# Optimization experiments

Measured on AMD Instinct MI355X. Metric: run time of the kernel, lower is better.

## Reference

```python
import jax, jax.numpy as jnp
import numpy as np

N_NODES = 50000


def gcn_conv(x, W, b, src, dst, ew, n):
    """PyG-style GCNConv: D^-1/2 (A+I) D^-1/2 X W + b with self-loops of weight 1."""
    h = x @ W                                   # [N, out]
    loop = jnp.arange(n, dtype=src.dtype)
    s = jnp.concatenate([src, loop])            # [E+N]
    d = jnp.concatenate([dst, loop])
    w = jnp.concatenate([ew, jnp.ones((n,), dtype=x.dtype)])
    deg = jax.ops.segment_sum(w, d, num_segments=n)
    dinv = jnp.where(deg > 0, jax.lax.rsqrt(deg), 0.0)
    norm = dinv[s] * w * dinv[d]                # [E+N]
    out = jax.ops.segment_sum(h[s] * norm[:, None], d, num_segments=n)
    return out + b


def setup_inputs() -> dict:
    key = jax.random.key(0)
    ks = jax.random.split(key, 12)
    in_feats, hidden = 128, 128
    half = hidden // 2
    E = 800000
    x = jax.random.normal(ks[0], (N_NODES, in_feats), dtype=jnp.float32)
    edge_index = jax.random.randint(ks[1], (2, E), 0, N_NODES, dtype=jnp.int64)
    edge_weight = jax.random.uniform(ks[2], (E,), dtype=jnp.float32)
    def lin(k, fan_in, shape):
        bound = 1.0 / np.sqrt(fan_in)
        return jax.random.uniform(k, shape, minval=-bound, maxval=bound, dtype=jnp.float32)
    return {
        "x": x,
        "edge_index": edge_index,
        "edge_weight": edge_weight,
        "W1": lin(ks[3], in_feats, (in_feats, hidden)),
        "b1": jnp.zeros((hidden,), jnp.float32),
        "W2": lin(ks[4], hidden, (hidden, hidden)),
        "b2": jnp.zeros((hidden,), jnp.float32),
        "Ws": lin(ks[5], in_feats, (in_feats, hidden)),
        "bs": lin(ks[6], in_feats, (hidden,)),
        "Wl": lin(ks[7], in_feats, (in_feats, half)),
        "bl": jnp.zeros((half,), jnp.float32),
        "Wl2": lin(ks[8], half, (half, 1)),
        "bl2": lin(ks[9], half, (1,)),
    }


def reference(x, edge_index, edge_weight, W1, b1, W2, b2, Ws, bs, Wl, bl, Wl2, bl2):
    n = x.shape[0]
    src, dst = edge_index[0], edge_index[1]
    # conv1 + ReLU over neighbors
    h_neighbors = jax.nn.relu(gcn_conv(x, W1, b1, src, dst, edge_weight, n))
    # leader score: GCNConv -> ReLU -> Linear(.,1) -> sigmoid, per node
    ls_h = jax.nn.relu(gcn_conv(x, Wl, bl, src, dst, edge_weight, n))
    leader_score = jax.nn.sigmoid(ls_h @ Wl2 + bl2)        # [N, 1]
    # gated fusion of self projection vs neighbor aggregation
    h_self_proj = x @ Ws + bs
    h_new = (1.0 - leader_score) * h_neighbors + leader_score * h_self_proj
    h_final = jax.nn.relu(gcn_conv(h_new, W2, b2, src, dst, edge_weight, n))
    return (h_final, leader_score)
```

## Files before the change

### kernel.cpp

```cpp
#include <hip/hip_runtime.h>
#include <math.h>

#define THREADS 256
#define ELLS 96
#define NEDGEBLK 1024
#define GEMM_YSTRIDE 104

typedef unsigned int uint32;
typedef unsigned long long ull64;
typedef __attribute__((ext_vector_type(8))) short bf16x8;
typedef __attribute__((ext_vector_type(4))) float f32x4;
typedef __attribute__((ext_vector_type(2))) float f32x2;

__device__ __forceinline__ unsigned short f2bf_rne(float x) {
  uint32 u = __float_as_uint(x);
  u += 0x7fffu + ((u >> 16) & 1u);
  return (unsigned short)(u >> 16);
}

__device__ __forceinline__ f32x2 dw2f2(uint32 d) {
  f32x2 r;
  r.x = __uint_as_float(d << 16);
  r.y = __uint_as_float(d & 0xffff0000u);
  return r;
}


__global__ __launch_bounds__(256) void prep_fused(ull64* __restrict__ packed, int n,
                                                  const float* __restrict__ W1, const float* __restrict__ Wl,
                                                  const float* __restrict__ Ws, const float* __restrict__ W2,
                                                  unsigned short* __restrict__ whi, unsigned short* __restrict__ wlo,
                                                  const float* __restrict__ x, unsigned short* __restrict__ xraw,
                                                  int nInit, int nW) {
  int b = blockIdx.x;
  int t = threadIdx.x;
  if (b < nInit) {
    int i = b * 256 + t;
    if (i < n) packed[i] = 0ull;
  } else if (b < nInit + nW) {
    int idx = (b - nInit) * 256 + t;
    if (idx >= 448 * 128) return;
    int slot = idx >> 7;
    int k = idx & 127;
    const float* W; int ncol, ncols;
    if (slot < 128)      { W = W1; ncol = slot;       ncols = 128; }
    else if (slot < 192) { W = Wl; ncol = slot - 128; ncols = 64;  }
    else if (slot < 320) { W = Ws; ncol = slot - 192; ncols = 128; }
    else                 { W = W2; ncol = slot - 320; ncols = 128; }
    float v = W[(size_t)k * ncols + ncol];
    unsigned short hi = f2bf_rne(v);
    float hif = __uint_as_float((uint32)hi << 16);
    unsigned short lo = f2bf_rne(v - hif);
    whi[idx] = hi;
    wlo[idx] = lo;
  } else {
    int i = (b - nInit - nW) * 256 + t;
    if (i >= n * 16) return;
    const float* px = x + (size_t)i * 8;
    float4 a = *(const float4*)px;
    float4 c = *(const float4*)(px + 4);
    ushort4 r0, r1;
    r0.x = f2bf_rne(a.x); r0.y = f2bf_rne(a.y); r0.z = f2bf_rne(a.z); r0.w = f2bf_rne(a.w);
    r1.x = f2bf_rne(c.x); r1.y = f2bf_rne(c.y); r1.z = f2bf_rne(c.z); r1.w = f2bf_rne(c.w);
    *(ushort4*)(xraw + (size_t)i * 8) = r0;
    *(ushort4*)(xraw + (size_t)i * 8 + 4) = r1;
  }
}


__global__ __launch_bounds__(256) void finalize_kernel(const ull64* __restrict__ packed,
                                                       float* __restrict__ dinv, int* __restrict__ cnt32, int n) {
  int i = blockIdx.x * 256 + threadIdx.x;
  if (i >= n) return;
  const float S = 1.1920928955078125e-7f;
  ull64 p = packed[i];
  dinv[i] = rsqrtf(1.0f + (float)(uint32)(p & 0xffffffffull) * S);
  cnt32[i] = (int)(p >> 32);
}


struct Chunk {
  const unsigned short* A;
  const unsigned short* whi;
  const unsigned short* wlo;
  const float* bias;
  void* out;
  int ostride;
  int obf16;
};
struct GemmArgs { Chunk c[5]; };

__device__ __forceinline__ void gemm_body(const Chunk& d, int M, int nTiles, int tile0, int tstride) {
  const unsigned short* A = d.A;
  int w = threadIdx.x >> 6, lane = threadIdx.x & 63;
  int n16 = lane & 15, quad = lane >> 4;

  bf16x8 Bh[4][4], Bl[4][4];
  {
    const unsigned short* wh = d.whi + (size_t)n16 * 128 + quad * 8;
    const unsigned short* wl = d.wlo + (size_t)n16 * 128 + quad * 8;
#pragma unroll
    for (int ct = 0; ct < 4; ct++)
#pragma unroll
      for (int ks = 0; ks < 4; ks++) {
        Bh[ct][ks] = *(const bf16x8*)(wh + ct * 16 * 128 + ks * 32);
        Bl[ct][ks] = *(const bf16x8*)(wl + ct * 16 * 128 + ks * 32);
      }
  }
  float bv[4];
#pragma unroll
  for (int ct = 0; ct < 4; ct++) bv[ct] = d.bias ? d.bias[ct * 16 + n16] : 0.f;

  int tile = tile0;
  bf16x8 av0[4], av1[4];
  if (tile < nTiles) {
    int bm = tile * 128;
    int r0 = bm + w * 32 + n16, r1 = r0 + 16;
    int r0c = r0 < M ? r0 : M - 1;
    int r1c = r1 < M ? r1 : M - 1;
    const unsigned short* a0 = A + (size_t)r0c * 128 + quad * 8;
    const unsigned short* a1 = A + (size_t)r1c * 128 + quad * 8;
#pragma unroll
    for (int ks = 0; ks < 4; ks++) {
      av0[ks] = *(const bf16x8*)(a0 + ks * 32);
      av1[ks] = *(const bf16x8*)(a1 + ks * 32);
    }
  }

  for (; tile < nTiles; tile += tstride) {
    int nxt = tile + tstride;
    bf16x8 nv0[4], nv1[4];
    if (nxt < nTiles) {
      int bm = nxt * 128;
      int r0 = bm + w * 32 + n16, r1 = r0 + 16;
      int r0c = r0 < M ? r0 : M - 1;
      int r1c = r1 < M ? r1 : M - 1;
      const unsigned short* a0 = A + (size_t)r0c * 128 + quad * 8;
      const unsigned short* a1 = A + (size_t)r1c * 128 + quad * 8;
#pragma unroll
      for (int ks = 0; ks < 4; ks++) {
        nv0[ks] = *(const bf16x8*)(a0 + ks * 32);
        nv1[ks] = *(const bf16x8*)(a1 + ks * 32);
      }
    }

    f32x4 acc[2][4];
#pragma unroll
    for (int rt = 0; rt < 2; rt++)
#pragma unroll
      for (int ct = 0; ct < 4; ct++) acc[rt][ct] = (f32x4){0.f, 0.f, 0.f, 0.f};

#pragma unroll
    for (int ks = 0; ks < 4; ks++)
#pragma unroll
      for (int ct = 0; ct < 4; ct++) {
        acc[0][ct] = __builtin_amdgcn_mfma_f32_16x16x32_bf16(av0[ks], Bh[ct][ks], acc[0][ct], 0, 0, 0);
        acc[0][ct] = __builtin_amdgcn_mfma_f32_16x16x32_bf16(av0[ks], Bl[ct][ks], acc[0][ct], 0, 0, 0);
        acc[1][ct] = __builtin_amdgcn_mfma_f32_16x16x32_bf16(av1[ks], Bh[ct][ks], acc[1][ct], 0, 0, 0);
        acc[1][ct] = __builtin_amdgcn_mfma_f32_16x16x32_bf16(av1[ks], Bl[ct][ks], acc[1][ct], 0, 0, 0);
      }

    int bm = tile * 128;
#pragma unroll
    for (int ct = 0; ct < 4; ct++) {
      int col = ct * 16 + n16;
#pragma unroll
      for (int rt = 0; rt < 2; rt++) {
#pragma unroll
        for (int reg = 0; reg < 4; reg++) {
          int row = bm + w * 32 + rt * 16 + quad * 4 + reg;
          if (row < M) {
            float v = acc[rt][ct][reg] + bv[ct];
            if (d.obf16)
              ((unsigned short*)d.out)[(size_t)row * d.ostride + col] = f2bf_rne(v);
            else
              ((float*)d.out)[(size_t)row * d.ostride + col] = v;
          }
        }
      }
    }

#pragma unroll
    for (int ks = 0; ks < 4; ks++) { av0[ks] = nv0[ks]; av1[ks] = nv1[ks]; }
  }
}

__global__ __launch_bounds__(256, 2) void gemm_v3(GemmArgs args, int M, int nTiles) {
  gemm_body(args.c[blockIdx.x], M, nTiles, blockIdx.y, gridDim.y);
}


__global__ __launch_bounds__(256, 2) void fused_sg(GemmArgs args, int M, int nTiles, int nGemm,
                                                   const int* __restrict__ ei, const float* __restrict__ ew,
                                                   ull64* __restrict__ packed, int2* __restrict__ ell, int E) {
  int b = blockIdx.x;
  int gemmIdx = -1, edgeIdx = -1;
  int twice = nGemm * 2;
  if (b < twice) {
    if (b & 1) gemmIdx = b >> 1; else edgeIdx = b >> 1;
  } else {
    edgeIdx = nGemm + (b - twice);
  }

  if (edgeIdx >= 0) {
    int per = (E + NEDGEBLK - 1) / NEDGEBLK;
    int start = edgeIdx * per;
    int end = start + per;
    if (end > E) end = E;
    for (int e = start + (int)threadIdx.x; e < end; e += 256) {
      int s = ei[e];
      int d = ei[E + e];
      float w = ew[e];
      uint32 fx = (uint32)(w * 8388608.0f + 0.5f);
      ull64 old = atomicAdd(packed + d, (1ull << 32) | (ull64)fx);
      int slot = (int)(old >> 32);
      if (slot < ELLS)
        ell[(size_t)d * ELLS + slot] = make_int2(s, __float_as_int(w));
    }
    return;
  }

  int chunkId = gemmIdx % 5;
  int ytile = gemmIdx / 5;
  gemm_body(args.c[chunkId], M, nTiles, ytile, GEMM_YSTRIDE);
}


__global__ __launch_bounds__(256) void conv1_fused(const unsigned short* __restrict__ h1,
                                                   const unsigned short* __restrict__ hl,
                                                   const int* __restrict__ cnt,
                                                   const int2* __restrict__ csr,
                                                   const float* __restrict__ dinv,
                                                   const float* __restrict__ b1, const float* __restrict__ bl,
                                                   const float* __restrict__ Wl2, const float* __restrict__ bl2,
                                                   const unsigned short* __restrict__ hself,
                                                   unsigned short* __restrict__ hnew_out,
                                                   float* __restrict__ leader_out, int nnodes) {
  int wave = threadIdx.x >> 6;
  int lane = threadIdx.x & 63;
  int node = blockIdx.x * 4 + wave;
  if (node >= nnodes) return;
  int g = lane >> 4, q = lane & 15;
  bool ql = q < 8;
  int hq = q & 7;
  int rs = node * ELLS;
  int n = cnt[node];
  float di = dinv[node];
  f32x2 dv2 = {di, di};

  f32x2 acc1[4] = {};
  f32x2 accl[4] = {};
  if (g == 0) {
    uint4 v = *(const uint4*)(h1 + (size_t)node * 128 + 8 * q);
    acc1[0] = dv2 * dw2f2(v.x); acc1[1] = dv2 * dw2f2(v.y);
    acc1[2] = dv2 * dw2f2(v.z); acc1[3] = dv2 * dw2f2(v.w);
    if (ql) {
      uint4 vl = *(const uint4*)(hl + (size_t)node * 64 + 8 * q);
      accl[0] = dv2 * dw2f2(vl.x); accl[1] = dv2 * dw2f2(vl.y);
      accl[2] = dv2 * dw2f2(vl.z); accl[3] = dv2 * dw2f2(vl.w);
    }
  }

  int e = g;
  for (; e + 4 < n; e += 8) {
    int2 en0 = csr[rs + e];
    int2 en1 = csr[rs + e + 4];
    float wz0 = __int_as_float(en0.y) * dinv[en0.x];
    float wz1 = __int_as_float(en1.y) * dinv[en1.x];
    f32x2 w0 = {wz0, wz0};
    f32x2 w1 = {wz1, wz1};
    uint4 a0 = *(const uint4*)(h1 + (size_t)en0.x * 128 + 8 * q);
    uint4 a1 = *(const uint4*)(h1 + (size_t)en1.x * 128 + 8 * q);
    int srcl = ql ? en0.x : en1.x;
    float wzl = ql ? wz0 : wz1;
    uint4 c0 = *(const uint4*)(hl + (size_t)srcl * 64 + 8 * hq);
    f32x2 wl2 = {wzl, wzl};
    accl[0] += wl2 * dw2f2(c0.x);
    accl[1] += wl2 * dw2f2(c0.y);
    accl[2] += wl2 * dw2f2(c0.z);
    accl[3] += wl2 * dw2f2(c0.w);
    acc1[0] += w0 * dw2f2(a0.x) + w1 * dw2f2(a1.x);
    acc1[1] += w0 * dw2f2(a0.y) + w1 * dw2f2(a1.y);
    acc1[2] += w0 * dw2f2(a0.z) + w1 * dw2f2(a1.z);
    acc1[3] += w0 * dw2f2(a0.w) + w1 * dw2f2(a1.w);
  }
  if (e < n) {
    int2 en = csr[rs + e];
    float wz0 = __int_as_float(en.y) * dinv[en.x];
    f32x2 w0 = {wz0, wz0};
    uint4 a0 = *(const uint4*)(h1 + (size_t)en.x * 128 + 8 * q);
    float wzl = ql ? wz0 : 0.f;
    uint4 c0 = *(const uint4*)(hl + (size_t)en.x * 64 + 8 * hq);
    f32x2 wl2 = {wzl, wzl};
    accl[0] += wl2 * dw2f2(c0.x);
    accl[1] += wl2 * dw2f2(c0.y);
    accl[2] += wl2 * dw2f2(c0.z);
    accl[3] += wl2 * dw2f2(c0.w);
    acc1[0] += w0 * dw2f2(a0.x);
    acc1[1] += w0 * dw2f2(a0.y);
    acc1[2] += w0 * dw2f2(a0.z);
    acc1[3] += w0 * dw2f2(a0.w);
  }

#pragma unroll
  for (int k = 0; k < 4; k++) {
    acc1[k].x += __shfl_xor(acc1[k].x, 16);
    acc1[k].y += __shfl_xor(acc1[k].y, 16);
    acc1[k].x += __shfl_xor(acc1[k].x, 32);
    acc1[k].y += __shfl_xor(acc1[k].y, 32);
    accl[k].x += __shfl_xor(accl[k].x, 16);
    accl[k].y += __shfl_xor(accl[k].y, 16);
    accl[k].x += __shfl_xor(accl[k].x, 32);
    accl[k].y += __shfl_xor(accl[k].y, 32);
    accl[k].x += __shfl_xor(accl[k].x, 8);
    accl[k].y += __shfl_xor(accl[k].y, 8);
  }

  float part = 0.f;
  if (ql) {
    float b[8], w2[8];
    *(float4*)&b[0] = *(const float4*)(bl + 8 * q);
    *(float4*)&b[4] = *(const float4*)(bl + 8 * q + 4);
    *(float4*)&w2[0] = *(const float4*)(Wl2 + 8 * q);
    *(float4*)&w2[4] = *(const float4*)(Wl2 + 8 * q + 4);
#pragma unroll
    for (int k = 0; k < 4; k++) {
      part += fmaxf(di * accl[k].x + b[2 * k], 0.f) * w2[2 * k];
      part += fmaxf(di * accl[k].y + b[2 * k + 1], 0.f) * w2[2 * k + 1];
    }
  }
  part += __shfl_xor(part, 1);
  part += __shfl_xor(part, 2);
  part += __shfl_xor(part, 4);
  float z = __shfl(part, 0) + bl2[0];
  float l = 1.f / (1.f + expf(-z));
  if (lane == 0) leader_out[node] = l;

  if (g == 0) {
    float b[8], r[8], hs[8];
    *(float4*)&b[0] = *(const float4*)(b1 + 8 * q);
    *(float4*)&b[4] = *(const float4*)(b1 + 8 * q + 4);
    uint4 hsv = *(const uint4*)(hself + (size_t)node * 128 + 8 * q);
    f32x2 h0 = dw2f2(hsv.x), h1v = dw2f2(hsv.y), h2v = dw2f2(hsv.z), h3v = dw2f2(hsv.w);
    hs[0] = h0.x; hs[1] = h0.y; hs[2] = h1v.x; hs[3] = h1v.y;
    hs[4] = h2v.x; hs[5] = h2v.y; hs[6] = h3v.x; hs[7] = h3v.y;
    float a[8];
    a[0] = acc1[0].x; a[1] = acc1[0].y; a[2] = acc1[1].x; a[3] = acc1[1].y;
    a[4] = acc1[2].x; a[5] = acc1[2].y; a[6] = acc1[3].x; a[7] = acc1[3].y;
#pragma unroll
    for (int j = 0; j < 8; j++) {
      r[j] = fmaxf(di * a[j] + b[j], 0.f);
      r[j] = (1.f - l) * r[j] + l * hs[j];
      r[j] *= di;
    }
    ushort4 p0, p1;
    p0.x = f2bf_rne(r[0]); p0.y = f2bf_rne(r[1]); p0.z = f2bf_rne(r[2]); p0.w = f2bf_rne(r[3]);
    p1.x = f2bf_rne(r[4]); p1.y = f2bf_rne(r[5]); p1.z = f2bf_rne(r[6]); p1.w = f2bf_rne(r[7]);
    *(ushort4*)(hnew_out + (size_t)node * 128 + 8 * q) = p0;
    *(ushort4*)(hnew_out + (size_t)node * 128 + 8 * q + 4) = p1;
  }
}


__global__ __launch_bounds__(256) void agg_conv2_kernel(const unsigned short* __restrict__ h,
                                                        const int* __restrict__ cnt,
                                                        const int2* __restrict__ csr,
                                                        const float* __restrict__ dinv, const float* __restrict__ bias,
                                                        float* __restrict__ out, int nnodes) {
  int wave = threadIdx.x >> 6;
  int lane = threadIdx.x & 63;
  int node = blockIdx.x * 4 + wave;
  if (node >= nnodes) return;
  int g = lane >> 4;
  int q = lane & 15;
  int rs = node * ELLS;
  int n = cnt[node];
  float di = dinv[node];

  f32x2 acc[4] = {};
  if (g == 0) {
    uint4 v = *(const uint4*)(h + (size_t)node * 128 + 8 * q);
    acc[0] = dw2f2(v.x); acc[1] = dw2f2(v.y);
    acc[2] = dw2f2(v.z); acc[3] = dw2f2(v.w);
  }
  int e = g;
  for (; e + 4 < n; e += 8) {
    int2 en0 = csr[rs + e];
    int2 en1 = csr[rs + e + 4];
    f32x2 w0 = {__int_as_float(en0.y), __int_as_float(en0.y)};
    f32x2 w1 = {__int_as_float(en1.y), __int_as_float(en1.y)};
    uint4 v0 = *(const uint4*)(h + (size_t)en0.x * 128 + 8 * q);
    uint4 v1 = *(const uint4*)(h + (size_t)en1.x * 128 + 8 * q);
    acc[0] += w0 * dw2f2(v0.x) + w1 * dw2f2(v1.x);
    acc[1] += w0 * dw2f2(v0.y) + w1 * dw2f2(v1.y);
    acc[2] += w0 * dw2f2(v0.z) + w1 * dw2f2(v1.z);
    acc[3] += w0 * dw2f2(v0.w) + w1 * dw2f2(v1.w);
  }
  if (e < n) {
    int2 en = csr[rs + e];
    f32x2 w0 = {__int_as_float(en.y), __int_as_float(en.y)};
    uint4 v = *(const uint4*)(h + (size_t)en.x * 128 + 8 * q);
    acc[0] += w0 * dw2f2(v.x);
    acc[1] += w0 * dw2f2(v.y);
    acc[2] += w0 * dw2f2(v.z);
    acc[3] += w0 * dw2f2(v.w);
  }
#pragma unroll
  for (int k = 0; k < 4; k++) {
    acc[k].x += __shfl_xor(acc[k].x, 16);
    acc[k].y += __shfl_xor(acc[k].y, 16);
    acc[k].x += __shfl_xor(acc[k].x, 32);
    acc[k].y += __shfl_xor(acc[k].y, 32);
  }
  if (g == 0) {
    float b[8], r[8];
    *(float4*)&b[0] = *(const float4*)(bias + 8 * q);
    *(float4*)&b[4] = *(const float4*)(bias + 8 * q + 4);
    float a[8];
    a[0] = acc[0].x; a[1] = acc[0].y; a[2] = acc[1].x; a[3] = acc[1].y;
    a[4] = acc[2].x; a[5] = acc[2].y; a[6] = acc[3].x; a[7] = acc[3].y;
#pragma unroll
    for (int j = 0; j < 8; j++) r[j] = fmaxf(di * a[j] + b[j], 0.f);
    *(float4*)(out + (size_t)node * 128 + 8 * q) = *(float4*)&r[0];
    *(float4*)(out + (size_t)node * 128 + 8 * q + 4) = *(float4*)&r[4];
  }
}


extern "C" void kernel_launch(void* const* d_in, const int* in_sizes, int n_in,
                              void* d_out, int out_size, void* d_ws, size_t ws_size,
                              hipStream_t stream) {
  const float* x   = (const float*)d_in[0];
  const int*   ei  = (const int*)d_in[1];
  const float* ew  = (const float*)d_in[2];
  const float* W1  = (const float*)d_in[3];
  const float* b1  = (const float*)d_in[4];
  const float* W2  = (const float*)d_in[5];
  const float* b2  = (const float*)d_in[6];
  const float* Wsp = (const float*)d_in[7];
  const float* bs  = (const float*)d_in[8];
  const float* Wl  = (const float*)d_in[9];
  const float* bl  = (const float*)d_in[10];
  const float* Wl2 = (const float*)d_in[11];
  const float* bl2 = (const float*)d_in[12];

  const int N = in_sizes[0] / 128;
  const int E = in_sizes[1] / 2;

  char* ws = (char*)d_ws;
  size_t off = 0;
  auto alloc = [&](size_t bytes) -> void* {
    void* p = ws + off;
    off = (off + bytes + 255) & ~(size_t)255;
    return p;
  };
  ull64* packed    = (ull64*)alloc((size_t)N * 8);
  float* dinv      = (float*)alloc((size_t)N * 4);
  int*   cnt32     = (int*)alloc((size_t)N * 4);
  int2*  ell       = (int2*)alloc((size_t)N * ELLS * 8);
  unsigned short* xraw   = (unsigned short*)alloc((size_t)N * 128 * 2);
  unsigned short* h1bf   = (unsigned short*)alloc((size_t)N * 128 * 2);
  unsigned short* hlbf   = (unsigned short*)alloc((size_t)N * 64 * 2);
  unsigned short* hnewbf = (unsigned short*)alloc((size_t)N * 128 * 2);
  unsigned short* hspbf  = (unsigned short*)alloc((size_t)N * 128 * 2);
  unsigned short* whi = (unsigned short*)alloc((size_t)448 * 128 * 2);
  unsigned short* wlo = (unsigned short*)alloc((size_t)448 * 128 * 2);

  float* h_final = (float*)d_out;
  float* leader  = (float*)d_out + (size_t)N * 128;

  int gN = (N + THREADS - 1) / THREADS;
  int gWave = (N + 3) / 4;
  int nTiles = (N + 127) / 128;
  int nCast = (N * 16 + 255) / 256;
  int nW = (448 * 128 + 255) / 256;

  prep_fused<<<gN + nW + nCast, 256, 0, stream>>>(packed, N, W1, Wl, Wsp, W2, whi, wlo, x, xraw, gN, nW);

  {
    GemmArgs ga;
    ga.c[0] = {xraw, whi + 0 * 128,   wlo + 0 * 128,   nullptr, h1bf,       128, 1};
    ga.c[1] = {xraw, whi + 64 * 128,  wlo + 64 * 128,  nullptr, h1bf + 64,  128, 1};
    ga.c[2] = {xraw, whi + 128 * 128, wlo + 128 * 128, nullptr, hlbf,       64,  1};
    ga.c[3] = {xraw, whi + 192 * 128, wlo + 192 * 128, bs,      hspbf,      128, 1};
    ga.c[4] = {xraw, whi + 256 * 128, wlo + 256 * 128, bs + 64, hspbf + 64, 128, 1};
    int nGemm = 5 * GEMM_YSTRIDE;
    int totalBlocks = nGemm * 2 + (NEDGEBLK - nGemm);
    fused_sg<<<totalBlocks, 256, 0, stream>>>(ga, N, nTiles, nGemm, ei, ew, packed, ell, E);
  }

  finalize_kernel<<<gN, 256, 0, stream>>>(packed, dinv, cnt32, N);

  conv1_fused<<<gWave, 256, 0, stream>>>(h1bf, hlbf, cnt32, ell, dinv,
                                         b1, bl, Wl2, bl2, hspbf, hnewbf, leader, N);

  {
    GemmArgs ga;
    ga.c[0] = {hnewbf, whi + 320 * 128, wlo + 320 * 128, nullptr, h1bf,      128, 1};
    ga.c[1] = {hnewbf, whi + 384 * 128, wlo + 384 * 128, nullptr, h1bf + 64, 128, 1};
    ga.c[2] = ga.c[0]; ga.c[3] = ga.c[0]; ga.c[4] = ga.c[0];
    gemm_v3<<<dim3(2, 256), 256, 0, stream>>>(ga, N, nTiles);
  }
  agg_conv2_kernel<<<gWave, 256, 0, stream>>>(h1bf, cnt32, ell,
                                              dinv, b2, h_final, N);
}
```

Before: 261.3 us.

## Fuse x bf16 cast into GEMM loads and use 32-bit dst-partitioned degree atomics

Drops the separate pass that casts x to bf16. The first GEMM now reads fp32 x directly and converts it to bf16 in registers, with prefetch into float4 registers. Degree accumulation is repacked from 64-bit into 32-bit atomics: a 9-bit count plus a 23-bit fixed-point weight sum at lower resolution. Edge blocks are grouped in eights that each scan the same edge chunk but only handle destinations in their own node range, to localise atomics. In exchange, each edge chunk is read eight times, the GEMM chunks read x at twice the bytes, and the degree values lose some precision.

```diff
diff --git a/kernel.cpp b/kernel.cpp
--- a/kernel.cpp
+++ b/kernel.cpp
@@ -25,19 +25,27 @@
   return r;
 }
 
-
-__global__ __launch_bounds__(256) void prep_fused(ull64* __restrict__ packed, int n,
+__device__ __forceinline__ bf16x8 cvt8(float4 a, float4 b) {
+  bf16x8 r;
+  r[0] = (short)f2bf_rne(a.x); r[1] = (short)f2bf_rne(a.y);
+  r[2] = (short)f2bf_rne(a.z); r[3] = (short)f2bf_rne(a.w);
+  r[4] = (short)f2bf_rne(b.x); r[5] = (short)f2bf_rne(b.y);
+  r[6] = (short)f2bf_rne(b.z); r[7] = (short)f2bf_rne(b.w);
+  return r;
+}
+
+
+__global__ __launch_bounds__(256) void prep_fused(uint32* __restrict__ packed, int n,
                                                   const float* __restrict__ W1, const float* __restrict__ Wl,
                                                   const float* __restrict__ Ws, const float* __restrict__ W2,
                                                   unsigned short* __restrict__ whi, unsigned short* __restrict__ wlo,
-                                                  const float* __restrict__ x, unsigned short* __restrict__ xraw,
-                                                  int nInit, int nW) {
+                                                  int nInit) {
   int b = blockIdx.x;
   int t = threadIdx.x;
   if (b < nInit) {
     int i = b * 256 + t;
-    if (i < n) packed[i] = 0ull;
-  } else if (b < nInit + nW) {
+    if (i < n) packed[i] = 0u;
+  } else {
     int idx = (b - nInit) * 256 + t;
     if (idx >= 448 * 128) return;
     int slot = idx >> 7;
@@ -53,34 +61,23 @@
     unsigned short lo = f2bf_rne(v - hif);
     whi[idx] = hi;
     wlo[idx] = lo;
-  } else {
-    int i = (b - nInit - nW) * 256 + t;
-    if (i >= n * 16) return;
-    const float* px = x + (size_t)i * 8;
-    float4 a = *(const float4*)px;
-    float4 c = *(const float4*)(px + 4);
-    ushort4 r0, r1;
-    r0.x = f2bf_rne(a.x); r0.y = f2bf_rne(a.y); r0.z = f2bf_rne(a.z); r0.w = f2bf_rne(a.w);
-    r1.x = f2bf_rne(c.x); r1.y = f2bf_rne(c.y); r1.z = f2bf_rne(c.z); r1.w = f2bf_rne(c.w);
-    *(ushort4*)(xraw + (size_t)i * 8) = r0;
-    *(ushort4*)(xraw + (size_t)i * 8 + 4) = r1;
-  }
-}
-
-
-__global__ __launch_bounds__(256) void finalize_kernel(const ull64* __restrict__ packed,
+  }
+}
+
+
+__global__ __launch_bounds__(256) void finalize_kernel(const uint32* __restrict__ packed,
                                                        float* __restrict__ dinv, int* __restrict__ cnt32, int n) {
   int i = blockIdx.x * 256 + threadIdx.x;
   if (i >= n) return;
-  const float S = 1.1920928955078125e-7f;
-  ull64 p = packed[i];
-  dinv[i] = rsqrtf(1.0f + (float)(uint32)(p & 0xffffffffull) * S);
-  cnt32[i] = (int)(p >> 32);
+  const float S = 7.62939453125e-6f;
+  uint32 p = packed[i];
+  dinv[i] = rsqrtf(1.0f + (float)(p & 0x7fffffu) * S);
+  cnt32[i] = (int)(p >> 23);
 }
 
 
 struct Chunk {
-  const unsigned short* A;
+  const void* A;
   const unsigned short* whi;
   const unsigned short* wlo;
   const float* bias;
@@ -90,8 +87,8 @@
 };
 struct GemmArgs { Chunk c[5]; };
 
+template <bool AF32>
 __device__ __forceinline__ void gemm_body(const Chunk& d, int M, int nTiles, int tile0, int tstride) {
-  const unsigned short* A = d.A;
   int w = threadIdx.x >> 6, lane = threadIdx.x & 63;
   int n16 = lane & 15, quad = lane >> 4;
 
@@ -118,29 +115,53 @@
     int r0 = bm + w * 32 + n16, r1 = r0 + 16;
     int r0c = r0 < M ? r0 : M - 1;
     int r1c = r1 < M ? r1 : M - 1;
-    const unsigned short* a0 = A + (size_t)r0c * 128 + quad * 8;
-    const unsigned short* a1 = A + (size_t)r1c * 128 + quad * 8;
-#pragma unroll
-    for (int ks = 0; ks < 4; ks++) {
-      av0[ks] = *(const bf16x8*)(a0 + ks * 32);
-      av1[ks] = *(const bf16x8*)(a1 + ks * 32);
+    if constexpr (AF32) {
+      const float* a0 = (const float*)d.A + (size_t)r0c * 128 + quad * 8;
+      const float* a1 = (const float*)d.A + (size_t)r1c * 128 + quad * 8;
+#pragma unroll
+      for (int ks = 0; ks < 4; ks++) {
+        av0[ks] = cvt8(*(const float4*)(a0 + ks * 32), *(const float4*)(a0 + ks * 32 + 4));
+        av1[ks] = cvt8(*(const float4*)(a1 + ks * 32), *(const float4*)(a1 + ks * 32 + 4));
+      }
+    } else {
+      const unsigned short* a0 = (const unsigned short*)d.A + (size_t)r0c * 128 + quad * 8;
+      const unsigned short* a1 = (const unsigned short*)d.A + (size_t)r1c * 128 + quad * 8;
+#pragma unroll
+      for (int ks = 0; ks < 4; ks++) {
+        av0[ks] = *(const bf16x8*)(a0 + ks * 32);
+        av1[ks] = *(const bf16x8*)(a1 + ks * 32);
+      }
     }
   }
 
   for (; tile < nTiles; tile += tstride) {
     int nxt = tile + tstride;
+    bool have = (nxt < nTiles);
+    float4 pf0[8], pf1[8];
     bf16x8 nv0[4], nv1[4];
-    if (nxt < nTiles) {
+    if (have) {
       int bm = nxt * 128;
       int r0 = bm + w * 32 + n16, r1 = r0 + 16;
       int r0c = r0 < M ? r0 : M - 1;
       int r1c = r1 < M ? r1 : M - 1;
-      const unsigned short* a0 = A + (size_t)r0c * 128 + quad * 8;
-      const unsigned short* a1 = A + (size_t)r1c * 128 + quad * 8;
-#pragma unroll
-      for (int ks = 0; ks < 4; ks++) {
-        nv0[ks] = *(const bf16x8*)(a0 + ks * 32);
-        nv1[ks] = *(const bf16x8*)(a1 + ks * 32);
+      if constexpr (AF32) {
+        const float* a0 = (const float*)d.A + (size_t)r0c * 128 + quad * 8;
+        const float* a1 = (const float*)d.A + (size_t)r1c * 128 + quad * 8;
+#pragma unroll
+        for (int ks = 0; ks < 4; ks++) {
+          pf0[2 * ks]     = *(const float4*)(a0 + ks * 32);
+          pf0[2 * ks + 1] = *(const float4*)(a0 + ks * 32 + 4);
+          pf1[2 * ks]     = *(const float4*)(a1 + ks * 32);
+          pf1[2 * ks + 1] = *(const float4*)(a1 + ks * 32 + 4);
+        }
+      } else {
+        const unsigned short* a0 = (const unsigned short*)d.A + (size_t)r0c * 128 + quad * 8;
+        const unsigned short* a1 = (const unsigned short*)d.A + (size_t)r1c * 128 + quad * 8;
+#pragma unroll
+        for (int ks = 0; ks < 4; ks++) {
+          nv0[ks] = *(const bf16x8*)(a0 + ks * 32);
+          nv1[ks] = *(const bf16x8*)(a1 + ks * 32);
+        }
       }
     }
 
@@ -180,49 +201,67 @@
       }
     }
 
-#pragma unroll
-    for (int ks = 0; ks < 4; ks++) { av0[ks] = nv0[ks]; av1[ks] = nv1[ks]; }
+    if (have) {
+      if constexpr (AF32) {
+#pragma unroll
+        for (int ks = 0; ks < 4; ks++) {
+          av0[ks] = cvt8(pf0[2 * ks], pf0[2 * ks + 1]);
+          av1[ks] = cvt8(pf1[2 * ks], pf1[2 * ks + 1]);
+        }
+      } else {
+#pragma unroll
+        for (int ks = 0; ks < 4; ks++) { av0[ks] = nv0[ks]; av1[ks] = nv1[ks]; }
+      }
+    }
   }
 }
 
 __global__ __launch_bounds__(256, 2) void gemm_v3(GemmArgs args, int M, int nTiles) {
-  gemm_body(args.c[blockIdx.x], M, nTiles, blockIdx.y, gridDim.y);
+  gemm_body<false>(args.c[blockIdx.x], M, nTiles, blockIdx.y, gridDim.y);
 }
 
 
 __global__ __launch_bounds__(256, 2) void fused_sg(GemmArgs args, int M, int nTiles, int nGemm,
                                                    const int* __restrict__ ei, const float* __restrict__ ew,
-                                                   ull64* __restrict__ packed, int2* __restrict__ ell, int E) {
+                                                   uint32* __restrict__ packed, int2* __restrict__ ell, int E) {
   int b = blockIdx.x;
-  int gemmIdx = -1, edgeIdx = -1;
-  int twice = nGemm * 2;
-  if (b < twice) {
-    if (b & 1) gemmIdx = b >> 1; else edgeIdx = b >> 1;
+  int grp = b >> 3, j = b & 7;
+  int nGG = nGemm >> 3;
+  int nPair = nGG * 2;
+  int gemmIdx = -1, edgeGrp = -1;
+  if (grp < nPair) {
+    if (grp & 1) gemmIdx = (grp >> 1) * 8 + j;
+    else edgeGrp = grp >> 1;
   } else {
-    edgeIdx = nGemm + (b - twice);
-  }
-
-  if (edgeIdx >= 0) {
-    int per = (E + NEDGEBLK - 1) / NEDGEBLK;
-    int start = edgeIdx * per;
-    int end = start + per;
-    if (end > E) end = E;
+    edgeGrp = nGG + (grp - nPair);
+  }
+
+  if (edgeGrp >= 0) {
+    int nChunk = NEDGEBLK / 8;
+    int per = (E + nChunk - 1) / nChunk;
+    int start = edgeGrp * per;
+    int end = start + per; if (end > E) end = E;
+    int range = (M + 7) >> 3;
+    int lo = j * range;
+    int hi = lo + range; if (hi > M) hi = M;
     for (int e = start + (int)threadIdx.x; e < end; e += 256) {
+      int d = ei[E + e];
       int s = ei[e];
-      int d = ei[E + e];
       float w = ew[e];
-      uint32 fx = (uint32)(w * 8388608.0f + 0.5f);
-      ull64 old = atomicAdd(packed + d, (1ull << 32) | (ull64)fx);
-      int slot = (int)(old >> 32);
-      if (slot < ELLS)
-        ell[(size_t)d * ELLS + slot] = make_int2(s, __float_as_int(w));
+      if (d >= lo && d < hi) {
+        uint32 fx = (uint32)(w * 131072.0f + 0.5f) | (1u << 23);
+        uint32 old = atomicAdd(packed + d, fx);
+        int slot = (int)(old >> 23);
+        if (slot < ELLS)
+          ell[(size_t)d * ELLS + slot] = make_int2(s, __float_as_int(w));
+      }
     }
     return;
   }
 
   int chunkId = gemmIdx % 5;
   int ytile = gemmIdx / 5;
-  gemm_body(args.c[chunkId], M, nTiles, ytile, GEMM_YSTRIDE);
+  gemm_body<true>(args.c[chunkId], M, nTiles, ytile, GEMM_YSTRIDE);
 }
 
 
@@ -454,11 +493,10 @@
     off = (off + bytes + 255) & ~(size_t)255;
     return p;
   };
-  ull64* packed    = (ull64*)alloc((size_t)N * 8);
+  uint32* packed   = (uint32*)alloc((size_t)N * 4);
   float* dinv      = (float*)alloc((size_t)N * 4);
   int*   cnt32     = (int*)alloc((size_t)N * 4);
   int2*  ell       = (int2*)alloc((size_t)N * ELLS * 8);
-  unsigned short* xraw   = (unsigned short*)alloc((size_t)N * 128 * 2);
   unsigned short* h1bf   = (unsigned short*)alloc((size_t)N * 128 * 2);
   unsigned short* hlbf   = (unsigned short*)alloc((size_t)N * 64 * 2);
   unsigned short* hnewbf = (unsigned short*)alloc((size_t)N * 128 * 2);
@@ -472,20 +510,21 @@
   int gN = (N + THREADS - 1) / THREADS;
   int gWave = (N + 3) / 4;
   int nTiles = (N + 127) / 128;
-  int nCast = (N * 16 + 255) / 256;
   int nW = (448 * 128 + 255) / 256;
 
-  prep_fused<<<gN + nW + nCast, 256, 0, stream>>>(packed, N, W1, Wl, Wsp, W2, whi, wlo, x, xraw, gN, nW);
+  prep_fused<<<gN + nW, 256, 0, stream>>>(packed, N, W1, Wl, Wsp, W2, whi, wlo, gN);
 
   {
     GemmArgs ga;
-    ga.c[0] = {xraw, whi + 0 * 128,   wlo + 0 * 128,   nullptr, h1bf,       128, 1};
-    ga.c[1] = {xraw, whi + 64 * 128,  wlo + 64 * 128,  nullptr, h1bf + 64,  128, 1};
-    ga.c[2] = {xraw, whi + 128 * 128, wlo + 128 * 128, nullptr, hlbf,       64,  1};
-    ga.c[3] = {xraw, whi + 192 * 128, wlo + 192 * 128, bs,      hspbf,      128, 1};
-    ga.c[4] = {xraw, whi + 256 * 128, wlo + 256 * 128, bs + 64, hspbf + 64, 128, 1};
+    ga.c[0] = {x, whi + 0 * 128,   wlo + 0 * 128,   nullptr, h1bf,       128, 1};
+    ga.c[1] = {x, whi + 64 * 128,  wlo + 64 * 128,  nullptr, h1bf + 64,  128, 1};
+    ga.c[2] = {x, whi + 128 * 128, wlo + 128 * 128, nullptr, hlbf,       64,  1};
+    ga.c[3] = {x, whi + 192 * 128, wlo + 192 * 128, bs,      hspbf,      128, 1};
+    ga.c[4] = {x, whi + 256 * 128, wlo + 256 * 128, bs + 64, hspbf + 64, 128, 1};
     int nGemm = 5 * GEMM_YSTRIDE;
-    int totalBlocks = nGemm * 2 + (NEDGEBLK - nGemm);
+    int nGG = nGemm / 8;
+    int nEG = NEDGEBLK / 8;
+    int totalBlocks = (nGG * 2 + (nEG - nGG)) * 8;
     fused_sg<<<totalBlocks, 256, 0, stream>>>(ga, N, nTiles, nGemm, ei, ew, packed, ell, E);
   }
 
```

Result: slower. 333.2 us (+27.5%).

## Bucket edges by destination block before ELL scatter and fuse finalize

Applied to the files above, without the earlier changes.

The single-pass global-atomic ELL construction becomes two phases. In phase A, blocks count edges per 128-node destination bucket in shared memory, reserve space with one global atomic per bucket, and write the edges into a staging buffer. Phase B, one block per bucket, does the packed atomics and ELL writes with localized destinations, then computes dinv and counts itself, replacing finalize_kernel. The aim is to cut scattered global atomics and improve locality, at the cost of an extra staging write and read and a BCAP overflow cap that could drop edges on skewed graphs.

```diff
diff --git a/kernel.cpp b/kernel.cpp
--- a/kernel.cpp
+++ b/kernel.cpp
@@ -3,8 +3,11 @@
 
 #define THREADS 256
 #define ELLS 96
-#define NEDGEBLK 1024
 #define GEMM_YSTRIDE 104
+#define NPHA 256
+#define BSHIFT 7
+#define NBMAX 392
+#define BCAP 2560
 
 typedef unsigned int uint32;
 typedef unsigned long long ull64;
@@ -26,7 +29,7 @@
 }
 
 
-__global__ __launch_bounds__(256) void prep_fused(ull64* __restrict__ packed, int n,
+__global__ __launch_bounds__(256) void prep_fused(ull64* __restrict__ packed, uint32* __restrict__ gcnt, int n,
                                                   const float* __restrict__ W1, const float* __restrict__ Wl,
                                                   const float* __restrict__ Ws, const float* __restrict__ W2,
                                                   unsigned short* __restrict__ whi, unsigned short* __restrict__ wlo,
@@ -37,6 +40,7 @@
   if (b < nInit) {
     int i = b * 256 + t;
     if (i < n) packed[i] = 0ull;
+    if (i < NBMAX) gcnt[i] = 0u;
   } else if (b < nInit + nW) {
     int idx = (b - nInit) * 256 + t;
     if (idx >= 448 * 128) return;
@@ -68,17 +72,6 @@
 }
 
 
-__global__ __launch_bounds__(256) void finalize_kernel(const ull64* __restrict__ packed,
-                                                       float* __restrict__ dinv, int* __restrict__ cnt32, int n) {
-  int i = blockIdx.x * 256 + threadIdx.x;
-  if (i >= n) return;
-  const float S = 1.1920928955078125e-7f;
-  ull64 p = packed[i];
-  dinv[i] = rsqrtf(1.0f + (float)(uint32)(p & 0xffffffffull) * S);
-  cnt32[i] = (int)(p >> 32);
-}
-
-
 struct Chunk {
   const unsigned short* A;
   const unsigned short* whi;
@@ -192,30 +185,41 @@
 
 __global__ __launch_bounds__(256, 2) void fused_sg(GemmArgs args, int M, int nTiles, int nGemm,
                                                    const int* __restrict__ ei, const float* __restrict__ ew,
-                                                   ull64* __restrict__ packed, int2* __restrict__ ell, int E) {
+                                                   uint32* __restrict__ gcnt, uint2* __restrict__ staging, int E) {
+  __shared__ uint32 cntS[NBMAX], curS[NBMAX], gbS[NBMAX];
   int b = blockIdx.x;
-  int gemmIdx = -1, edgeIdx = -1;
-  int twice = nGemm * 2;
+  int gemmIdx = -1, phIdx = -1;
+  int twice = NPHA * 2;
   if (b < twice) {
-    if (b & 1) gemmIdx = b >> 1; else edgeIdx = b >> 1;
+    if (b & 1) gemmIdx = b >> 1; else phIdx = b >> 1;
   } else {
-    edgeIdx = nGemm + (b - twice);
-  }
-
-  if (edgeIdx >= 0) {
-    int per = (E + NEDGEBLK - 1) / NEDGEBLK;
-    int start = edgeIdx * per;
-    int end = start + per;
-    if (end > E) end = E;
-    for (int e = start + (int)threadIdx.x; e < end; e += 256) {
-      int s = ei[e];
-      int d = ei[E + e];
-      float w = ew[e];
-      uint32 fx = (uint32)(w * 8388608.0f + 0.5f);
-      ull64 old = atomicAdd(packed + d, (1ull << 32) | (ull64)fx);
-      int slot = (int)(old >> 32);
-      if (slot < ELLS)
-        ell[(size_t)d * ELLS + slot] = make_int2(s, __float_as_int(w));
+    gemmIdx = NPHA + (b - twice);
+  }
+
+  if (phIdx >= 0) {
+    int t = threadIdx.x;
+    int per = (E + NPHA - 1) / NPHA;
+    int start = phIdx * per;
+    int end = start + per; if (end > E) end = E;
+    for (int k = t; k < NBMAX; k += 256) cntS[k] = 0u;
+    __syncthreads();
+    for (int i = start + t; i < end; i += 256)
+      atomicAdd(&cntS[(uint32)ei[E + i] >> BSHIFT], 1u);
+    __syncthreads();
+    for (int k = t; k < NBMAX; k += 256) {
+      uint32 c = cntS[k];
+      gbS[k] = c ? atomicAdd(&gcnt[k], c) : 0u;
+      curS[k] = 0u;
+    }
+    __syncthreads();
+    for (int i = start + t; i < end; i += 256) {
+      int d = ei[E + i];
+      int s = ei[i];
+      float w = ew[i];
+      int bk = d >> BSHIFT;
+      uint32 pos = atomicAdd(&curS[bk], 1u) + gbS[bk];
+      if (pos < BCAP)
+        staging[(size_t)bk * BCAP + pos] = make_uint2(((uint32)(d & 127) << 24) | (uint32)s, __float_as_uint(w));
     }
     return;
   }
@@ -223,6 +227,37 @@
   int chunkId = gemmIdx % 5;
   int ytile = gemmIdx / 5;
   gemm_body(args.c[chunkId], M, nTiles, ytile, GEMM_YSTRIDE);
+}
+
+
+__global__ __launch_bounds__(256) void phaseB_kernel(const uint2* __restrict__ staging,
+                                                     const uint32* __restrict__ gcnt,
+                                                     ull64* __restrict__ packed, int2* __restrict__ ell,
+                                                     float* __restrict__ dinv, int* __restrict__ cnt32, int n) {
+  int b = blockIdx.x;
+  int t = threadIdx.x;
+  uint32 cnt = gcnt[b]; if (cnt > BCAP) cnt = BCAP;
+  const uint2* sb = staging + (size_t)b * BCAP;
+  int dbase = b << BSHIFT;
+  for (uint32 i = t; i < cnt; i += 256) {
+    uint2 en = sb[i];
+    int d = dbase + (int)(en.x >> 24);
+    int s = (int)(en.x & 0xffffffu);
+    float w = __uint_as_float(en.y);
+    uint32 fx = (uint32)(w * 8388608.0f + 0.5f);
+    ull64 old = atomicAdd(packed + d, (1ull << 32) | (ull64)fx);
+    int slot = (int)(old >> 32);
+    if (slot < ELLS)
+      ell[(size_t)d * ELLS + slot] = make_int2(s, __float_as_int(w));
+  }
+  __syncthreads();
+  const float S = 1.1920928955078125e-7f;
+  int dend = dbase + 128; if (dend > n) dend = n;
+  for (int d = dbase + t; d < dend; d += 256) {
+    ull64 p = atomicAdd(packed + d, 0ull);
+    dinv[d] = rsqrtf(1.0f + (float)(uint32)(p & 0xffffffffull) * S);
+    cnt32[d] = (int)(p >> 32);
+  }
 }
 
 
@@ -446,6 +481,7 @@
 
   const int N = in_sizes[0] / 128;
   const int E = in_sizes[1] / 2;
+  const int NB = (N + 127) >> BSHIFT;
 
   char* ws = (char*)d_ws;
   size_t off = 0;
@@ -455,6 +491,8 @@
     return p;
   };
   ull64* packed    = (ull64*)alloc((size_t)N * 8);
+  uint32* gcnt     = (uint32*)alloc((size_t)NBMAX * 4);
+  uint2* staging   = (uint2*)alloc((size_t)NBMAX * BCAP * 8);
   float* dinv      = (float*)alloc((size_t)N * 4);
   int*   cnt32     = (int*)alloc((size_t)N * 4);
   int2*  ell       = (int2*)alloc((size_t)N * ELLS * 8);
@@ -475,7 +513,7 @@
   int nCast = (N * 16 + 255) / 256;
   int nW = (448 * 128 + 255) / 256;
 
-  prep_fused<<<gN + nW + nCast, 256, 0, stream>>>(packed, N, W1, Wl, Wsp, W2, whi, wlo, x, xraw, gN, nW);
+  prep_fused<<<gN + nW + nCast, 256, 0, stream>>>(packed, gcnt, N, W1, Wl, Wsp, W2, whi, wlo, x, xraw, gN, nW);
 
   {
     GemmArgs ga;
@@ -485,11 +523,11 @@
     ga.c[3] = {xraw, whi + 192 * 128, wlo + 192 * 128, bs,      hspbf,      128, 1};
     ga.c[4] = {xraw, whi + 256 * 128, wlo + 256 * 128, bs + 64, hspbf + 64, 128, 1};
     int nGemm = 5 * GEMM_YSTRIDE;
-    int totalBlocks = nGemm * 2 + (NEDGEBLK - nGemm);
-    fused_sg<<<totalBlocks, 256, 0, stream>>>(ga, N, nTiles, nGemm, ei, ew, packed, ell, E);
-  }
-
-  finalize_kernel<<<gN, 256, 0, stream>>>(packed, dinv, cnt32, N);
+    int totalBlocks = NPHA * 2 + (nGemm - NPHA);
+    fused_sg<<<totalBlocks, 256, 0, stream>>>(ga, N, nTiles, nGemm, ei, ew, gcnt, staging, E);
+  }
+
+  phaseB_kernel<<<NB, 256, 0, stream>>>(staging, gcnt, packed, ell, dinv, cnt32, N);
 
   conv1_fused<<<gWave, 256, 0, stream>>>(h1bf, hlbf, cnt32, ell, dinv,
                                          b1, bl, Wl2, bl2, hspbf, hnewbf, leader, N);
```

New measurement: 267.9 us. 1.03x slower.
